# Performance work log

Hardware: AMD Instinct MI355X
Metric: run time of the kernel (lower is better)

## Reference

```python
import jax, jax.numpy as jnp
import numpy as np

B, T, E, H, L = 2, 2048, 1024, 16, 4
HD = E // H
FF = 4 * E


def setup_inputs() -> dict:
    key = jax.random.key(0)
    ks = jax.random.split(key, 9)
    s = 0.02
    return {
        "x": jax.random.normal(ks[0], (B, T, E), dtype=jnp.float32),
        "Wqkv": jax.random.normal(ks[1], (L, E, 3 * E), dtype=jnp.float32) * s,
        "bqkv": jnp.zeros((L, 3 * E), dtype=jnp.float32),
        "Wproj": jax.random.normal(ks[2], (L, E, E), dtype=jnp.float32) * s,
        "bproj": jnp.zeros((L, E), dtype=jnp.float32),
        "W1": jax.random.normal(ks[3], (L, E, FF), dtype=jnp.float32) * s,
        "b1": jnp.zeros((L, FF), dtype=jnp.float32),
        "W2": jax.random.normal(ks[4], (L, FF, E), dtype=jnp.float32) * s,
        "b2": jnp.zeros((L, E), dtype=jnp.float32),
    }


def _attention(x, Wqkv_l, bqkv_l, Wproj_l, bproj_l):
    # (B,T,E) -> (B,T,E); manual softmax attention as in source
    qkv = x @ Wqkv_l + bqkv_l                      # (B,T,3E)
    q, k, v = jnp.split(qkv, 3, axis=-1)
    q = q.reshape(B, T, H, HD).transpose(0, 2, 1, 3)  # (B,H,T,HD)
    k = k.reshape(B, T, H, HD).transpose(0, 2, 1, 3)
    v = v.reshape(B, T, H, HD).transpose(0, 2, 1, 3)
    att = jnp.einsum("bhqd,bhkd->bhqk", q, k) * (1.0 / np.sqrt(HD))
    att = jax.nn.softmax(att, axis=-1)             # (B,H,T,T)
    y = jnp.einsum("bhqk,bhkd->bhqd", att, v)      # (B,H,T,HD)
    y = y.transpose(0, 2, 1, 3).reshape(B, T, E)
    return y @ Wproj_l + bproj_l


def reference(x, Wqkv, bqkv, Wproj, bproj, W1, b1, W2, b2):
    for l in range(L):
        x = x + _attention(x, Wqkv[l], bqkv[l], Wproj[l], bproj[l])  # residual x+f(x)
        h = jax.nn.gelu(x @ W1[l] + b1[l]) @ W2[l] + b2[l]           # MLP block
        x = x + h
    return x
```

## Files before the change

kernel.cpp:

```cpp
#include <hip/hip_runtime.h>
#include <hip/hip_bf16.h>

#define B_  2
#define T_  2048
#define E_  1024
#define H_  16
#define HD_ 64
#define FF_ 4096
#define L_  4
#define M_  (B_*T_)
#define RS_ (3*E_)

typedef unsigned short u16;
typedef __attribute__((ext_vector_type(8))) short  short8;
typedef __attribute__((ext_vector_type(4))) float  f32x4;

#define QS 0.18033688011112042f

__device__ __forceinline__ u16 f2bf(float f) {
    union { float f; unsigned u; } v; v.f = f;
    unsigned r = (v.u + 0x7fffu + ((v.u >> 16) & 1u)) >> 16;
    return (u16)r;
}
__device__ __forceinline__ u16 f2bf_trunc(float f) {
    union { float f; unsigned u; } v; v.f = f;
    return (u16)(v.u >> 16);
}

__device__ __forceinline__ void gll16(const u16* g, u16* lds) {
    __builtin_amdgcn_global_load_lds(
        (const __attribute__((address_space(1))) unsigned int*)g,
        (__attribute__((address_space(3))) unsigned int*)lds, 16, 0, 0);
}

__global__ __launch_bounds__(256) void transpose_weights(
    const float* __restrict__ Wqkv, const float* __restrict__ Wproj,
    const float* __restrict__ W1,   const float* __restrict__ W2,
    u16* __restrict__ WT) {
    __shared__ float tile[32][33];
    int bid = blockIdx.x;
    const float* src; u16* dst; int K, N, lt;
    if (bid < 3072)      { src = Wqkv;  dst = WT;           K = 1024; N = 3072; lt = bid;        }
    else if (bid < 4096) { src = Wproj; dst = WT + 3145728; K = 1024; N = 1024; lt = bid - 3072; }
    else if (bid < 8192) { src = W1;    dst = WT + 4194304; K = 1024; N = 4096; lt = bid - 4096; }
    else                 { src = W2;    dst = WT + 8388608; K = 4096; N = 1024; lt = bid - 8192; }
    int tpr = N >> 5;
    int ti = lt / tpr, tj = lt % tpr;
    int k0 = ti << 5, n0 = tj << 5;
    int tx = threadIdx.x & 31, ty = threadIdx.x >> 5;
    for (int i = 0; i < 4; i++) {
        int r = ty + (i << 3);
        tile[r][tx] = src[(size_t)(k0 + r) * N + n0 + tx];
    }
    __syncthreads();
    for (int i = 0; i < 4; i++) {
        int r = ty + (i << 3);
        dst[(size_t)(n0 + r) * K + k0 + tx] = f2bf(tile[tx][r]);
    }
}

__global__ __launch_bounds__(256) void convert_kernel(
    const float* __restrict__ in, u16* __restrict__ out, int n4) {
    int i = blockIdx.x * 256 + threadIdx.x;
    if (i < n4) {
        float4 v = ((const float4*)in)[i];
        ushort4 w;
        w.x = f2bf(v.x); w.y = f2bf(v.y); w.z = f2bf(v.z); w.w = f2bf(v.w);
        ((ushort4*)out)[i] = w;
    }
}

template <int EPI>
__global__ __launch_bounds__(256) void gemm_kernel(
    const u16* __restrict__ A, const u16* __restrict__ Bt,
    const float* __restrict__ bias, void* outp, int M, int N, int K) {
    __shared__ u16 As[2][128 * 32];
    __shared__ u16 Bs[2][128 * 32];
    int t = threadIdx.x;
    int wid = t >> 6, lane = t & 63;
    int m0 = blockIdx.y << 7, n0 = blockIdx.x << 7;
    int l15 = t & 15, quad = (t >> 4) & 3;
    int wr = wid >> 1, wc = wid & 1;
    f32x4 acc[4][4];
#pragma unroll
    for (int i = 0; i < 4; i++)
#pragma unroll
        for (int j = 0; j < 4; j++) acc[i][j] = (f32x4){0.f, 0.f, 0.f, 0.f};

    int srow = (wid << 5) + (lane >> 2);
    int kch  = (((lane & 3) ^ ((lane >> 3) & 3)) << 3);
    const u16* gA = &A [(size_t)(m0 + srow) * K + kch];
    const u16* gB = &Bt[(size_t)(n0 + srow) * K + kch];
    int xo = (l15 >> 1) & 3;
    int abase = (((wr << 6) + l15) << 5) + ((quad ^ xo) << 3);
    int bbase = (((wc << 6) + l15) << 5) + ((quad ^ xo) << 3);

    int nk = K >> 5;
#pragma unroll
    for (int g = 0; g < 2; g++) {
        gll16(gA + (size_t)(g << 4) * K, &As[0][((wid << 5) + (g << 4)) << 5]);
        gll16(gB + (size_t)(g << 4) * K, &Bs[0][((wid << 5) + (g << 4)) << 5]);
    }
    for (int kk = 0; kk < nk; kk++) {
        __syncthreads();
        const u16* as = &As[kk & 1][0];
        const u16* bs = &Bs[kk & 1][0];
        if (kk + 1 < nk) {
            int k1 = (kk + 1) << 5;
            int bn = (kk + 1) & 1;
#pragma unroll
            for (int g = 0; g < 2; g++) {
                gll16(gA + (size_t)(g << 4) * K + k1, &As[bn][((wid << 5) + (g << 4)) << 5]);
                gll16(gB + (size_t)(g << 4) * K + k1, &Bs[bn][((wid << 5) + (g << 4)) << 5]);
            }
        }
        short8 af[4], bf[4];
#pragma unroll
        for (int i = 0; i < 4; i++)
            af[i] = *(const short8*)(as + abase + (i << 9));
#pragma unroll
        for (int j = 0; j < 4; j++)
            bf[j] = *(const short8*)(bs + bbase + (j << 9));
#pragma unroll
        for (int i = 0; i < 4; i++)
#pragma unroll
            for (int j = 0; j < 4; j++)
                acc[i][j] = __builtin_amdgcn_mfma_f32_16x16x32_bf16(af[i], bf[j], acc[i][j], 0, 0, 0);
    }
#pragma unroll
    for (int j = 0; j < 4; j++) {
        int gn = (n0 + (wc << 6) + (j << 4)) + l15;
        float bv = bias[gn];
#pragma unroll
        for (int i = 0; i < 4; i++) {
            int mb = m0 + (wr << 6) + (i << 4) + (quad << 2);
#pragma unroll
            for (int r = 0; r < 4; r++) {
                size_t idx = (size_t)(mb + r) * N + gn;
                float v = acc[i][j][r] + bv;
                if (EPI == 0) {
                    if (gn < E_) v *= QS;
                    ((u16*)outp)[idx] = f2bf(v);
                } else {
                    float u  = 0.7978845608028654f * (v + 0.044715f * v * v * v);
                    float th = 1.f - 2.f / (__expf(2.f * u) + 1.f);
                    ((u16*)outp)[idx] = f2bf(0.5f * v * (1.f + th));
                }
            }
        }
    }
}

__global__ __launch_bounds__(256) void gemm_n64(
    const u16* __restrict__ A, const u16* __restrict__ Bt,
    const float* __restrict__ bias, const float* __restrict__ res,
    float* __restrict__ outp, u16* __restrict__ out2, int M, int N, int K) {
    __shared__ u16 As[2][128 * 64];
    __shared__ u16 Bs[2][64 * 64];
    int t = threadIdx.x;
    int wid = t >> 6, lane = t & 63;
    int m0 = blockIdx.y << 7, n0 = blockIdx.x << 6;
    int l15 = t & 15, quad = (t >> 4) & 3;
    int wr = wid >> 1, wc = wid & 1;
    f32x4 acc[4][2];
#pragma unroll
    for (int i = 0; i < 4; i++)
#pragma unroll
        for (int j = 0; j < 2; j++) acc[i][j] = (f32x4){0.f, 0.f, 0.f, 0.f};

    int srow = lane >> 3;
    int kch  = (((lane & 7) ^ srow) << 3);
    const u16* gA = &A [(size_t)(m0 + (wid << 5) + srow) * K + kch];
    const u16* gB = &Bt[(size_t)(n0 + (wid << 4) + srow) * K + kch];
    int xo = l15 & 7;

    int nk = K >> 6;
#pragma unroll
    for (int g = 0; g < 4; g++)
        gll16(gA + (size_t)(g << 3) * K, &As[0][((wid << 5) + (g << 3)) << 6]);
#pragma unroll
    for (int g = 0; g < 2; g++)
        gll16(gB + (size_t)(g << 3) * K, &Bs[0][((wid << 4) + (g << 3)) << 6]);

    for (int kk = 0; kk < nk; kk++) {
        __syncthreads();
        int b = kk & 1;
        if (kk + 1 < nk) {
            int k1 = (kk + 1) << 6;
#pragma unroll
            for (int g = 0; g < 4; g++)
                gll16(gA + (size_t)(g << 3) * K + k1, &As[b ^ 1][((wid << 5) + (g << 3)) << 6]);
#pragma unroll
            for (int g = 0; g < 2; g++)
                gll16(gB + (size_t)(g << 3) * K + k1, &Bs[b ^ 1][((wid << 4) + (g << 3)) << 6]);
        }
        short8 af[2][4], bf[2][2];
#pragma unroll
        for (int kq = 0; kq < 2; kq++) {
            int ch = (((kq << 2) | quad) ^ xo) << 3;
#pragma unroll
            for (int i = 0; i < 4; i++)
                af[kq][i] = *(const short8*)&As[b][((wr << 6) + (i << 4) + l15) * 64 + ch];
#pragma unroll
            for (int j = 0; j < 2; j++)
                bf[kq][j] = *(const short8*)&Bs[b][((wc << 5) + (j << 4) + l15) * 64 + ch];
        }
#pragma unroll
        for (int kq = 0; kq < 2; kq++)
#pragma unroll
            for (int i = 0; i < 4; i++)
#pragma unroll
                for (int j = 0; j < 2; j++)
                    acc[i][j] = __builtin_amdgcn_mfma_f32_16x16x32_bf16(
                        af[kq][i], bf[kq][j], acc[i][j], 0, 0, 0);
    }
#pragma unroll
    for (int j = 0; j < 2; j++) {
        int gn = n0 + (wc << 5) + (j << 4) + l15;
        float bv = bias[gn];
#pragma unroll
        for (int i = 0; i < 4; i++) {
            int mb = m0 + (wr << 6) + (i << 4) + (quad << 2);
#pragma unroll
            for (int r = 0; r < 4; r++) {
                size_t idx = (size_t)(mb + r) * N + gn;
                float o = acc[i][j][r] + bv + res[idx];
                outp[idx] = o;
                out2[idx] = f2bf(o);
            }
        }
    }
}

__global__ __launch_bounds__(256) void attn_kernel(
    const u16* __restrict__ qkv, u16* __restrict__ y) {
    __shared__ u16 Ks[2][64 * 64];
    __shared__ u16 Vt[2][64 * 64];
    __shared__ u16 Pb[4][16 * 64];

    int t = threadIdx.x;
    int q0 = blockIdx.x << 6;
    int h  = blockIdx.y;
    int b  = blockIdx.z;
    const u16* bq = qkv + (size_t)b * T_ * RS_;

    int wid = t >> 6, lane = t & 63, l15 = t & 15, quad = (t >> 4) & 3;
    int sw = l15 & 7;
    int ro0 = (l15 << 6) + ((quad ^ sw) << 3);
    int ro1 = ro0 ^ 32;
    int krow = (wid << 4) + (lane >> 3);
    size_t kg0 = (size_t)krow * RS_ + E_ + h * 64 + (((lane & 7) ^ (lane >> 3)) << 3);
    int vkp = t & 31, vdc = t >> 5;
    size_t vg0 = (size_t)(2 * vkp) * RS_ + 2 * E_ + h * 64 + (vdc << 3);
    int vwo[8];
#pragma unroll
    for (int i = 0; i < 8; i++)
        vwo[i] = (((vdc << 3) + i) << 6) + ((((vkp >> 2) ^ i)) << 3) + ((vkp & 3) << 1);
    int pwo[4];
#pragma unroll
    for (int kt = 0; kt < 4; kt++)
        pwo[kt] = (l15 << 6) + ((((kt << 1) | (quad >> 1)) ^ sw) << 3) + ((quad & 1) << 2);
    u16* pw = &Pb[wid][0];

    const u16* qp = bq + (size_t)(q0 + (wid << 4) + l15) * RS_ + h * 64;
    short8 qf0 = *(const short8*)(qp + (quad << 3));
    short8 qf1 = *(const short8*)(qp + (quad << 3) + 32);

    float m = -1e30f, l = 0.f;
    f32x4 o[4];
#pragma unroll
    for (int dt = 0; dt < 4; dt++) o[dt] = (f32x4){0.f, 0.f, 0.f, 0.f};

    gll16(bq + kg0,            &Ks[0][(wid << 4) << 6]);
    gll16(bq + kg0 + 8 * RS_,  &Ks[0][((wid << 4) + 8) << 6]);
    {
        union { uint4 q; u16 u[8]; } a_, b_;
        a_.q = *(const uint4*)(bq + vg0);
        b_.q = *(const uint4*)(bq + vg0 + RS_);
#pragma unroll
        for (int i = 0; i < 8; i++) {
            unsigned pk = (unsigned)a_.u[i] | ((unsigned)b_.u[i] << 16);
            *(unsigned*)(&Vt[0][0] + vwo[i]) = pk;
        }
    }

#define ATTN_CHUNK(KSB, VTB, KSN, VTN, C0) do {                                \
    __syncthreads();                           \
    int cn_ = (C0) + 64;                                                       \
    uint4 v0_, v1_;                                                            \
    bool pf_ = (cn_ < T_);                                                     \
    if (pf_) {                                                                 \
        size_t cb_ = (size_t)cn_ * RS_;                                        \
        gll16(bq + cb_ + kg0,           (KSN) + ((wid << 4) << 6));            \
        gll16(bq + cb_ + kg0 + 8 * RS_, (KSN) + (((wid << 4) + 8) << 6));      \
        v0_ = *(const uint4*)(bq + cb_ + vg0);                                 \
        v1_ = *(const uint4*)(bq + cb_ + vg0 + RS_);                           \
    }                                                                          \
    f32x4 s_[4];                                                               \
    _Pragma("unroll")                                                          \
    for (int kt = 0; kt < 4; kt++) {                                           \
        short8 ka0 = *(const short8*)((KSB) + (kt << 10) + ro0);               \
        short8 ka1 = *(const short8*)((KSB) + (kt << 10) + ro1);               \
        f32x4 z = (f32x4){0.f, 0.f, 0.f, 0.f};                                 \
        z = __builtin_amdgcn_mfma_f32_16x16x32_bf16(ka0, qf0, z, 0, 0, 0);     \
        z = __builtin_amdgcn_mfma_f32_16x16x32_bf16(ka1, qf1, z, 0, 0, 0);     \
        s_[kt] = z;                                                            \
    }                                                                          \
    float cm_ = -1e30f;                                                        \
    _Pragma("unroll")                                                          \
    for (int kt = 0; kt < 4; kt++)                                             \
        _Pragma("unroll")                                                      \
        for (int r = 0; r < 4; r++) cm_ = fmaxf(cm_, s_[kt][r]);               \
    cm_ = fmaxf(cm_, __shfl_xor(cm_, 16));                                     \
    cm_ = fmaxf(cm_, __shfl_xor(cm_, 32));                                     \
    float mn_ = fmaxf(m, cm_);                                                 \
    float alpha_ = __builtin_amdgcn_exp2f(m - mn_);                            \
    float rsum_ = 0.f;                                                         \
    _Pragma("unroll")                                                          \
    for (int kt = 0; kt < 4; kt++) {                                           \
        float p0_ = __builtin_amdgcn_exp2f(s_[kt][0] - mn_);                   \
        float p1_ = __builtin_amdgcn_exp2f(s_[kt][1] - mn_);                   \
        float p2_ = __builtin_amdgcn_exp2f(s_[kt][2] - mn_);                   \
        float p3_ = __builtin_amdgcn_exp2f(s_[kt][3] - mn_);                   \
        rsum_ += (p0_ + p1_) + (p2_ + p3_);                                    \
        ushort4 w_;                                                            \
        w_.x = f2bf_trunc(p0_); w_.y = f2bf_trunc(p1_);                        \
        w_.z = f2bf_trunc(p2_); w_.w = f2bf_trunc(p3_);                        \
        *(ushort4*)(pw + pwo[kt]) = w_;                                        \
    }                                                                          \
    rsum_ += __shfl_xor(rsum_, 16);                                            \
    rsum_ += __shfl_xor(rsum_, 32);                                            \
    l = l * alpha_ + rsum_;                                                    \
    m = mn_;                                                                   \
    __threadfence_block();                   \
    short8 pb0 = *(const short8*)(pw + ro0);                                   \
    short8 pb1 = *(const short8*)(pw + ro1);                                   \
    _Pragma("unroll")                                                          \
    for (int dt = 0; dt < 4; dt++) {                                           \
        _Pragma("unroll")                                                      \
        for (int r = 0; r < 4; r++) o[dt][r] *= alpha_;                        \
        short8 vf0 = *(const short8*)((VTB) + (dt << 10) + ro0);               \
        short8 vf1 = *(const short8*)((VTB) + (dt << 10) + ro1);               \
        o[dt] = __builtin_amdgcn_mfma_f32_16x16x32_bf16(vf0, pb0, o[dt], 0, 0, 0); \
        o[dt] = __builtin_amdgcn_mfma_f32_16x16x32_bf16(vf1, pb1, o[dt], 0, 0, 0); \
    }                                                                          \
    if (pf_) {                                                                 \
        union { uint4 q; u16 u[8]; } a_, b_;                                   \
        a_.q = v0_; b_.q = v1_;                                                \
        _Pragma("unroll")                                                      \
        for (int i = 0; i < 8; i++) {                                          \
            unsigned pk_ = (unsigned)a_.u[i] | ((unsigned)b_.u[i] << 16);      \
            *(unsigned*)((VTN) + vwo[i]) = pk_;                                \
        }                                                                      \
    }                                                                          \
} while (0)

    for (int c0 = 0; c0 < T_; c0 += 128) {
        ATTN_CHUNK(&Ks[0][0], &Vt[0][0], &Ks[1][0], &Vt[1][0], c0);
        ATTN_CHUNK(&Ks[1][0], &Vt[1][0], &Ks[0][0], &Vt[0][0], c0 + 64);
    }
#undef ATTN_CHUNK

    float rl = __builtin_amdgcn_rcpf(l);
    size_t yrow = ((size_t)b * T_ + q0 + (wid << 4) + l15) * E_ + h * 64;
#pragma unroll
    for (int dt = 0; dt < 4; dt++) {
        ushort4 w;
        w.x = f2bf(o[dt][0] * rl); w.y = f2bf(o[dt][1] * rl);
        w.z = f2bf(o[dt][2] * rl); w.w = f2bf(o[dt][3] * rl);
        *(ushort4*)&y[yrow + (dt << 4) + (quad << 2)] = w;
    }
}

extern "C" void kernel_launch(void* const* d_in, const int* in_sizes, int n_in,
                              void* d_out, int out_size, void* d_ws, size_t ws_size,
                              hipStream_t stream) {
    const float* x_in  = (const float*)d_in[0];
    const float* Wqkv  = (const float*)d_in[1];
    const float* bqkv  = (const float*)d_in[2];
    const float* Wproj = (const float*)d_in[3];
    const float* bproj = (const float*)d_in[4];
    const float* W1    = (const float*)d_in[5];
    const float* b1    = (const float*)d_in[6];
    const float* W2    = (const float*)d_in[7];
    const float* b2    = (const float*)d_in[8];
    float* out = (float*)d_out;

    u16* WT   = (u16*)d_ws;
    u16* qkvb = WT   + 12582912;
    u16* yb   = qkvb + 12582912;
    u16* hb   = yb   + 4194304;
    u16* xb   = hb   + 16777216;

    convert_kernel<<<4096, 256, 0, stream>>>(x_in, xb, M_ * E_ / 4);

    for (int l = 0; l < L_; l++) {
        transpose_weights<<<12288, 256, 0, stream>>>(
            Wqkv + (size_t)l * E_ * 3 * E_, Wproj + (size_t)l * E_ * E_,
            W1 + (size_t)l * E_ * FF_, W2 + (size_t)l * FF_ * E_, WT);

        const float* xcur = (l == 0) ? x_in : out;

        gemm_kernel<0><<<dim3(24, 32), 256, 0, stream>>>(
            xb, WT, bqkv + l * 3 * E_, qkvb, M_, 3 * E_, E_);

        attn_kernel<<<dim3(T_ / 64, H_, B_), 256, 0, stream>>>(qkvb, yb);

        gemm_n64<<<dim3(16, 32), 256, 0, stream>>>(
            yb, WT + 3145728, bproj + l * E_, xcur, out, xb, M_, E_, E_);

        gemm_kernel<2><<<dim3(32, 32), 256, 0, stream>>>(
            xb, WT + 4194304, b1 + l * FF_, hb, M_, FF_, E_);

        gemm_n64<<<dim3(16, 32), 256, 0, stream>>>(
            hb, WT + 8388608, b2 + l * E_, out, out, xb, M_, E_, FF_);
    }
}
```

Baseline: 1.197 ms.

## Use 128x256 tiles with triple-buffered loads and XCD-aware block swizzle

Replaces the 128x128 GEMM for the QKV and FC1 projections with a 512-thread 128x256 tile kernel. It uses a three-stage LDS ring with explicit vmcnt waits, so one barrier per k-step can overlap two tiles of loads. Both GEMM kernels now remap flat block ids to spread neighbouring tiles across the 8 XCDs and group 4 N-tiles per M-stripe for L2 reuse. The new kernel uses more LDS and relies on hand-written waitcnt counts matching the number of loads issued per stage.

```diff
diff --git a/kernel.cpp b/kernel.cpp
--- a/kernel.cpp
+++ b/kernel.cpp
@@ -71,65 +71,81 @@
 }
 
 template <int EPI>
-__global__ __launch_bounds__(256) void gemm_kernel(
+__global__ __launch_bounds__(512, 4) void gemm_fat(
     const u16* __restrict__ A, const u16* __restrict__ Bt,
-    const float* __restrict__ bias, void* outp, int M, int N, int K) {
-    __shared__ u16 As[2][128 * 32];
-    __shared__ u16 Bs[2][128 * 32];
+    const float* __restrict__ bias, u16* __restrict__ outp,
+    int N, int K) {
+    __shared__ u16 As[3][128 * 32];
+    __shared__ u16 Bs[3][256 * 32];
     int t = threadIdx.x;
     int wid = t >> 6, lane = t & 63;
-    int m0 = blockIdx.y << 7, n0 = blockIdx.x << 7;
     int l15 = t & 15, quad = (t >> 4) & 3;
-    int wr = wid >> 1, wc = wid & 1;
+    int wr = wid >> 2, wc = wid & 3;
+
+    int nbx = N >> 8;
+    int nwg = nbx << 5;
+    int flat = blockIdx.x;
+    int q = nwg >> 3;
+    int gid = (flat & 7) * q + (flat >> 3);
+    int within = gid & 127;
+    int m0 = (within >> 2) << 7;
+    int n0 = (((gid >> 7) << 2) + (within & 3)) << 8;
+
     f32x4 acc[4][4];
 #pragma unroll
     for (int i = 0; i < 4; i++)
 #pragma unroll
         for (int j = 0; j < 4; j++) acc[i][j] = (f32x4){0.f, 0.f, 0.f, 0.f};
 
-    int srow = (wid << 5) + (lane >> 2);
+    int srow = t >> 2;
     int kch  = (((lane & 3) ^ ((lane >> 3) & 3)) << 3);
-    const u16* gA = &A [(size_t)(m0 + srow) * K + kch];
-    const u16* gB = &Bt[(size_t)(n0 + srow) * K + kch];
+    const u16* gA  = &A [(size_t)(m0 + srow) * K + kch];
+    const u16* gB0 = &Bt[(size_t)(n0 + srow) * K + kch];
+    const u16* gB1 = gB0 + (size_t)128 * K;
+
     int xo = (l15 >> 1) & 3;
     int abase = (((wr << 6) + l15) << 5) + ((quad ^ xo) << 3);
     int bbase = (((wc << 6) + l15) << 5) + ((quad ^ xo) << 3);
 
     int nk = K >> 5;
-#pragma unroll
-    for (int g = 0; g < 2; g++) {
-        gll16(gA + (size_t)(g << 4) * K, &As[0][((wid << 5) + (g << 4)) << 5]);
-        gll16(gB + (size_t)(g << 4) * K, &Bs[0][((wid << 5) + (g << 4)) << 5]);
-    }
+
+#define STAGE_FAT(buf, ko) do {                                              \
+        gll16(gA  + (ko), &As[buf][(wid << 4) << 5]);                        \
+        gll16(gB0 + (ko), &Bs[buf][(wid << 4) << 5]);                        \
+        gll16(gB1 + (ko), &Bs[buf][((wid << 4) + 128) << 5]);                \
+    } while (0)
+
+    STAGE_FAT(0, 0);
+    STAGE_FAT(1, 32);
+
     for (int kk = 0; kk < nk; kk++) {
-        __syncthreads();
-        const u16* as = &As[kk & 1][0];
-        const u16* bs = &Bs[kk & 1][0];
-        if (kk + 1 < nk) {
-            int k1 = (kk + 1) << 5;
-            int bn = (kk + 1) & 1;
-#pragma unroll
-            for (int g = 0; g < 2; g++) {
-                gll16(gA + (size_t)(g << 4) * K + k1, &As[bn][((wid << 5) + (g << 4)) << 5]);
-                gll16(gB + (size_t)(g << 4) * K + k1, &Bs[bn][((wid << 5) + (g << 4)) << 5]);
-            }
-        }
-        short8 af[4], bf[4];
+        if (kk < nk - 1) asm volatile("s_waitcnt vmcnt(3)" ::: "memory");
+        else             asm volatile("s_waitcnt vmcnt(0)" ::: "memory");
+        __builtin_amdgcn_s_barrier();
+        __builtin_amdgcn_sched_barrier(0);
+
+        if (kk + 2 < nk) STAGE_FAT((kk + 2) % 3, (kk + 2) << 5);
+
+        const u16* as = &As[kk % 3][0];
+        const u16* bs = &Bs[kk % 3][0];
+        short8 af[4], bfr[4];
 #pragma unroll
         for (int i = 0; i < 4; i++)
             af[i] = *(const short8*)(as + abase + (i << 9));
 #pragma unroll
         for (int j = 0; j < 4; j++)
-            bf[j] = *(const short8*)(bs + bbase + (j << 9));
+            bfr[j] = *(const short8*)(bs + bbase + (j << 9));
 #pragma unroll
         for (int i = 0; i < 4; i++)
 #pragma unroll
             for (int j = 0; j < 4; j++)
-                acc[i][j] = __builtin_amdgcn_mfma_f32_16x16x32_bf16(af[i], bf[j], acc[i][j], 0, 0, 0);
-    }
+                acc[i][j] = __builtin_amdgcn_mfma_f32_16x16x32_bf16(af[i], bfr[j], acc[i][j], 0, 0, 0);
+    }
+#undef STAGE_FAT
+
 #pragma unroll
     for (int j = 0; j < 4; j++) {
-        int gn = (n0 + (wc << 6) + (j << 4)) + l15;
+        int gn = n0 + (wc << 6) + (j << 4) + l15;
         float bv = bias[gn];
 #pragma unroll
         for (int i = 0; i < 4; i++) {
@@ -140,11 +156,11 @@
                 float v = acc[i][j][r] + bv;
                 if (EPI == 0) {
                     if (gn < E_) v *= QS;
-                    ((u16*)outp)[idx] = f2bf(v);
+                    outp[idx] = f2bf(v);
                 } else {
                     float u  = 0.7978845608028654f * (v + 0.044715f * v * v * v);
                     float th = 1.f - 2.f / (__expf(2.f * u) + 1.f);
-                    ((u16*)outp)[idx] = f2bf(0.5f * v * (1.f + th));
+                    outp[idx] = f2bf(0.5f * v * (1.f + th));
                 }
             }
         }
@@ -159,7 +175,11 @@
     __shared__ u16 Bs[2][64 * 64];
     int t = threadIdx.x;
     int wid = t >> 6, lane = t & 63;
-    int m0 = blockIdx.y << 7, n0 = blockIdx.x << 6;
+    int flat = blockIdx.y * gridDim.x + blockIdx.x;
+    int gid = ((flat & 7) << 6) + (flat >> 3);
+    int within = gid & 127;
+    int m0 = (within >> 2) << 7;
+    int n0 = (((gid >> 7) << 2) + (within & 3)) << 6;
     int l15 = t & 15, quad = (t >> 4) & 3;
     int wr = wid >> 1, wc = wid & 1;
     f32x4 acc[4][2];
@@ -401,16 +421,16 @@
 
         const float* xcur = (l == 0) ? x_in : out;
 
-        gemm_kernel<0><<<dim3(24, 32), 256, 0, stream>>>(
-            xb, WT, bqkv + l * 3 * E_, qkvb, M_, 3 * E_, E_);
+        gemm_fat<0><<<dim3(384), 512, 0, stream>>>(
+            xb, WT, bqkv + l * 3 * E_, qkvb, 3 * E_, E_);
 
         attn_kernel<<<dim3(T_ / 64, H_, B_), 256, 0, stream>>>(qkvb, yb);
 
         gemm_n64<<<dim3(16, 32), 256, 0, stream>>>(
             yb, WT + 3145728, bproj + l * E_, xcur, out, xb, M_, E_, E_);
 
-        gemm_kernel<2><<<dim3(32, 32), 256, 0, stream>>>(
-            xb, WT + 4194304, b1 + l * FF_, hb, M_, FF_, E_);
+        gemm_fat<2><<<dim3(512), 512, 0, stream>>>(
+            xb, WT + 4194304, b1 + l * FF_, hb, FF_, E_);
 
         gemm_n64<<<dim3(16, 32), 256, 0, stream>>>(
             hb, WT + 8388608, b2 + l * E_, out, out, xb, M_, E_, FF_);
```

After: 1.147 ms. -4.2%, faster.
